# Kernel tuning notes

Hardware: AMD Instinct MI355X
Metric: run time of the kernel (lower is better)

Reference implementation:

```python
import jax, jax.numpy as jnp
import numpy as np

B, L, C, V = 16, 600, 256, 256
OUT_SEQ = 6000
KSZ = 5
DILATIONS = (1, 2, 4)
N_BLOCKS = 10
COND = 256  # speaker(128) + noise(128)
TEMP = 10.0
EPS = 1e-5


def _ccbn(x, cond, gw, gb, bw, bb):
    # x: (B, C, L); conditional batch-norm: per-channel stats over (batch, length),
    # gamma/beta predicted from condition vector.
    mu = jnp.mean(x, axis=(0, 2), keepdims=True)
    var = jnp.var(x, axis=(0, 2), keepdims=True)
    xn = (x - mu) * jax.lax.rsqrt(var + EPS)
    gamma = 1.0 + cond @ gw + gb  # (B, C)
    beta = cond @ bw + bb         # (B, C)
    return xn * gamma[:, :, None] + beta[:, :, None]


def _conv1d(x, w, b, dil=1):
    # x: (B, C_in, L); w: (C_out, C_in, K)
    y = jax.lax.conv_general_dilated(
        x, w, window_strides=(1,), padding='SAME', rhs_dilation=(dil,),
        dimension_numbers=('NCH', 'OIH', 'NCH'))
    return y + b[None, :, None]


def setup_inputs() -> dict:
    key = jax.random.key(0)
    ks = jax.random.split(key, 20)
    s = 0.02
    inp = {
        'inputs': jax.random.randint(ks[0], (B, L), 0, V),
        'speaker_embeddings': jax.random.normal(ks[1], (B, 128), jnp.float32),
        'noise': jax.random.normal(ks[2], (B, 128), jnp.float32),
        'emb': jax.random.normal(ks[3], (V, C), jnp.float32) * s,
        # 10 blocks x 3 dilated convs
        'conv_w': jax.random.normal(ks[4], (N_BLOCKS, 3, C, C, KSZ), jnp.float32) * s,
        'conv_b': jnp.zeros((N_BLOCKS, 3, C), jnp.float32),
        # CCBN projections per conv (gamma/beta from condition)
        'g_w': jax.random.normal(ks[5], (N_BLOCKS, 3, COND, C), jnp.float32) * s,
        'g_b': jnp.zeros((N_BLOCKS, 3, C), jnp.float32),
        'b_w': jax.random.normal(ks[6], (N_BLOCKS, 3, COND, C), jnp.float32) * s,
        'b_b': jnp.zeros((N_BLOCKS, 3, C), jnp.float32),
        # TokenLength head: 2 CCBNs + conv1 (256->256,k1) + conv2 (256->1,k1)
        'tl_g_w': jax.random.normal(ks[7], (2, COND, C), jnp.float32) * s,
        'tl_g_b': jnp.zeros((2, C), jnp.float32),
        'tl_b_w': jax.random.normal(ks[8], (2, COND, C), jnp.float32) * s,
        'tl_b_b': jnp.zeros((2, C), jnp.float32),
        'tl_conv1_w': jax.random.normal(ks[9], (C, C, 1), jnp.float32) * s,
        'tl_conv1_b': jnp.zeros((C,), jnp.float32),
        'tl_conv2_w': jax.random.normal(ks[10], (1, C, 1), jnp.float32) * s,
        'tl_conv2_b': jnp.zeros((1,), jnp.float32),
    }
    return inp


def reference(inputs, speaker_embeddings, noise, emb, conv_w, conv_b,
              g_w, g_b, b_w, b_b, tl_g_w, tl_g_b, tl_b_w, tl_b_b,
              tl_conv1_w, tl_conv1_b, tl_conv2_w, tl_conv2_b):
    cond = jnp.concatenate([speaker_embeddings, noise], axis=-1)  # (B, COND)
    x = emb[inputs]                    # (B, L, C)
    x = jnp.transpose(x, (0, 2, 1))    # (B, C, L)

    # 10 unaligned blocks: residual stacks of CCBN -> ReLU -> dilated conv
    for blk in range(N_BLOCKS):
        y = x
        for j, d in enumerate(DILATIONS):
            y = jax.nn.relu(_ccbn(y, cond, g_w[blk, j], g_b[blk, j], b_w[blk, j], b_b[blk, j]))
            y = _conv1d(y, conv_w[blk, j], conv_b[blk, j], dil=d)
        x = x + y
    unaligned = x  # (B, C, L)

    # TokenLength head
    t = jax.nn.relu(_ccbn(unaligned, cond, tl_g_w[0], tl_g_b[0], tl_b_w[0], tl_b_b[0]))
    t = _conv1d(t, tl_conv1_w, tl_conv1_b)
    t = jax.nn.relu(_ccbn(t, cond, tl_g_w[1], tl_g_b[1], tl_b_w[1], tl_b_b[1]))
    t = _conv1d(t, tl_conv2_w, tl_conv2_b)  # (B, 1, L)
    token_lengths = jax.nn.relu(t[:, 0, :])  # (B, L)

    token_ends = jnp.cumsum(token_lengths, axis=-1)        # (B, L)
    token_centers = token_ends - token_lengths / 2.0        # (B, L)
    aligned_lengths = token_ends

    out_pos = jnp.arange(OUT_SEQ, dtype=jnp.float32)         # (OUT,)
    diff = token_centers[:, None, :] - out_pos[None, :, None]  # (B, OUT, L)
    logits = -(diff * diff) / TEMP
    weights = jax.nn.softmax(logits, axis=-1)                # (B, OUT, L)

    feats = jnp.transpose(unaligned, (0, 2, 1))              # (B, L, C)
    aligned_features = jnp.einsum('bol,blc->boc', weights, feats)  # (B, OUT, C)
    return aligned_features, aligned_lengths
```

## Files before the change

### kernel.cpp

```cpp
#include <hip/hip_runtime.h>
#include <math.h>

#define EPSv 1e-5f

typedef short short8 __attribute__((ext_vector_type(8)));
typedef float floatx4 __attribute__((ext_vector_type(4)));

__device__ __forceinline__ unsigned short f2bf(float x) {
  unsigned u = __float_as_uint(x);
  unsigned r = (u + 0x7fffu + ((u >> 16) & 1u)) >> 16;
  return (unsigned short)r;
}

__global__ void k_zero(float* __restrict__ p) {
  p[blockIdx.x * 256 + threadIdx.x] = 0.f;
}

__global__ void k_gamma_beta(const float* __restrict__ spk, const float* __restrict__ noise,
                             const float* __restrict__ g_w, const float* __restrict__ g_b,
                             const float* __restrict__ b_w, const float* __restrict__ b_b,
                             const float* __restrict__ tl_g_w, const float* __restrict__ tl_g_b,
                             const float* __restrict__ tl_b_w, const float* __restrict__ tl_b_b,
                             float* __restrict__ gammas, float* __restrict__ betas) {
  __shared__ float condl[16*256];
  int t = threadIdx.x;
  for (int idx = t; idx < 4096; idx += 256) {
    int b = idx >> 8, k = idx & 255;
    condl[idx] = (k < 128) ? spk[b*128 + k] : noise[b*128 + k - 128];
  }
  __syncthreads();
  int i = blockIdx.x;
  const float *gw, *bw, *gbias, *bbias;
  if (i < 30) { gw = g_w + (size_t)i*65536; bw = b_w + (size_t)i*65536; gbias = g_b + i*256; bbias = b_b + i*256; }
  else { int j = i - 30; gw = tl_g_w + (size_t)j*65536; bw = tl_b_w + (size_t)j*65536; gbias = tl_g_b + j*256; bbias = tl_b_b + j*256; }
  int co = (t & 63) + blockIdx.y * 64;
  int slot = t >> 6;
  float g[4] = {0.f,0.f,0.f,0.f}, bt[4] = {0.f,0.f,0.f,0.f};
  for (int k = 0; k < 256; ++k) {
    float gwv = gw[k*256 + co];
    float bwv = bw[k*256 + co];
    #pragma unroll
    for (int bb = 0; bb < 4; ++bb) {
      float cv = condl[(slot*4 + bb)*256 + k];
      g[bb]  = fmaf(cv, gwv, g[bb]);
      bt[bb] = fmaf(cv, bwv, bt[bb]);
    }
  }
  #pragma unroll
  for (int bb = 0; bb < 4; ++bb) {
    int b = slot*4 + bb;
    gammas[i*4096 + b*256 + co] = 1.0f + g[bb] + gbias[co];
    betas [i*4096 + b*256 + co] = bt[bb] + bbias[co];
  }
}

template<int TAPS>
__device__ __forceinline__ void wprep_body(const float* __restrict__ src,
                                           unsigned short* __restrict__ dst,
                                           int cotile, int chunk, int t) {
  int cow = t >> 2, ci8 = (t & 3) * 8;
  const float* s0 = src + ((size_t)(cotile*64 + cow)*256 + chunk*32 + ci8)*TAPS;
  float v[8*TAPS];
  #pragma unroll
  for (int i = 0; i < 8*TAPS; ++i) v[i] = s0[i];
  unsigned short* dblk = dst + (size_t)cotile*(8*TAPS*4096) + (size_t)chunk*(TAPS*4096);
  #pragma unroll
  for (int tap = 0; tap < TAPS; ++tap) {
    unsigned hi2[4], lo2[4];
    #pragma unroll
    for (int jj = 0; jj < 4; ++jj) {
      float a = v[(jj*2+0)*TAPS + tap], b = v[(jj*2+1)*TAPS + tap];
      unsigned short ha = f2bf(a), hb = f2bf(b);
      unsigned short la = f2bf(a - __uint_as_float((unsigned)ha << 16));
      unsigned short lb = f2bf(b - __uint_as_float((unsigned)hb << 16));
      hi2[jj] = (unsigned)ha | ((unsigned)hb << 16);
      lo2[jj] = (unsigned)la | ((unsigned)lb << 16);
    }
    uint4 H; H.x = hi2[0]; H.y = hi2[1]; H.z = hi2[2]; H.w = hi2[3];
    uint4 L; L.x = lo2[0]; L.y = lo2[1]; L.z = lo2[2]; L.w = lo2[3];
    *(uint4*)(dblk + (size_t)(tap*2)*2048 + cow*32 + ci8) = H;
    *(uint4*)(dblk + (size_t)(tap*2+1)*2048 + cow*32 + ci8) = L;
  }
}

__global__ __launch_bounds__(256) void k_wprep(const float* __restrict__ conv_w,
                                               const float* __restrict__ tl_c1_w,
                                               unsigned short* __restrict__ wp) {
  int cc = blockIdx.x;
  int cotile = blockIdx.y >> 3, chunk = blockIdx.y & 7;
  if (cc == 30) wprep_body<1>(tl_c1_w, wp + (size_t)30*655360, cotile, chunk, threadIdx.x);
  else          wprep_body<5>(conv_w + (size_t)cc*327680, wp + (size_t)cc*655360, cotile, chunk, threadIdx.x);
}

__global__ void k_embed2(const int* __restrict__ inp, const float* __restrict__ emb,
                         float* __restrict__ x, float* __restrict__ stat0) {
  int bx = blockIdx.x;
  int c = threadIdx.x;
  int r0 = bx * 60;
  float s = 0.f, s2 = 0.f;
  for (int r = 0; r < 60; ++r) {
    int row = inp[r0 + r];
    float v = emb[(size_t)row*256 + c];
    x[(size_t)(r0 + r)*256 + c] = v;
    s += v; s2 = fmaf(v, v, s2);
  }
  atomicAdd(&stat0[c], s);
  atomicAdd(&stat0[256 + c], s2);
}

template<int TAPS>
__global__ __launch_bounds__(256) void k_convm(const float* __restrict__ zin, float* __restrict__ out,
                        const float* __restrict__ stat_in, float* __restrict__ stat_out,
                        const float* __restrict__ gam, const float* __restrict__ bet,
                        const unsigned short* __restrict__ wpc,
                        const float* __restrict__ bias, int dil, int mode) {
  __shared__ unsigned short Zhi[3200];
  __shared__ unsigned short Zlo[3200];
  __shared__ float s_sc[256];
  __shared__ float s_sh[256];
  __shared__ float lsum[32];
  __shared__ float lsq[32];
  int t = threadIdx.x;
  int bx = blockIdx.x;
  int b  = bx / 10;
  int l0 = (bx % 10) * 64;
  int co0 = blockIdx.y * 32;
  int cobase = (blockIdx.y & 1) * 32;
  int PAD = ((TAPS - 1)/2) * dil;
  int ROWS = 64 + 2*PAD;
  int w = t >> 6, lane = t & 63;
  int lsub = (w & 1) * 32, cosub = (w >> 1) * 16;
  int quad = lane >> 4, nlan = lane & 15;
  if (t < 32) { lsum[t] = 0.f; lsq[t] = 0.f; }
  {
    float s = stat_in[t], s2 = stat_in[256 + t];
    float mu = s * (1.0f/9600.0f);
    float var = s2 * (1.0f/9600.0f) - mu*mu;
    float rs = rsqrtf(var + EPSv);
    float scale = rs * gam[b*256 + t];
    s_sc[t] = scale;
    s_sh[t] = fmaf(-mu, scale, bet[b*256 + t]);
  }

  floatx4 acc[2];
  acc[0] = (floatx4){0.f,0.f,0.f,0.f};
  acc[1] = (floatx4){0.f,0.f,0.f,0.f};

  const float* zb = zin + (size_t)b*600*256;
  int srow = t >> 3, fq = t & 7;
  int ar0 = (lsub + nlan) * 40 + quad * 8;
  int ar1 = (lsub + 16 + nlan) * 40 + quad * 8;

  bool va[3]; long zbase[3];
  #pragma unroll
  for (int i = 0; i < 3; ++i) {
    int r = srow + i*32;
    int gl = l0 - PAD + r;
    va[i] = (r < ROWS) && (gl >= 0) && (gl < 600);
    zbase[i] = (long)gl*256 + fq*4;
  }

  for (int chunk = 0; chunk < 8; ++chunk) {
    int ci0 = chunk * 32;
    const unsigned short* pch = wpc + (size_t)((blockIdx.y >> 1)*8 + chunk) * (TAPS*4096);
    short8 bh[TAPS], bl[TAPS];
    int cw = (cobase + cosub + nlan)*32 + quad*8;
    #pragma unroll
    for (int tap = 0; tap < TAPS; ++tap) {
      bh[tap] = *(const short8*)(pch + (size_t)(tap*2)*2048 + cw);
      bl[tap] = *(const short8*)(pch + (size_t)(tap*2+1)*2048 + cw);
    }
    float4 zr[3];
    #pragma unroll
    for (int i = 0; i < 3; ++i) {
      float4 z = {0.f,0.f,0.f,0.f};
      if (va[i]) z = *(const float4*)&zb[zbase[i] + ci0];
      zr[i] = z;
    }
    __syncthreads();
    float4 sc4 = *(const float4*)&s_sc[ci0 + fq*4];
    float4 sh4 = *(const float4*)&s_sh[ci0 + fq*4];
    #pragma unroll
    for (int i = 0; i < 3; ++i) {
      int r = srow + i*32;
      if (r < ROWS) {
        float4 z = zr[i];
        bool inr = va[i];
        float v0 = inr ? fmaxf(fmaf(z.x, sc4.x, sh4.x), 0.f) : 0.f;
        float v1 = inr ? fmaxf(fmaf(z.y, sc4.y, sh4.y), 0.f) : 0.f;
        float v2 = inr ? fmaxf(fmaf(z.z, sc4.z, sh4.z), 0.f) : 0.f;
        float v3 = inr ? fmaxf(fmaf(z.w, sc4.w, sh4.w), 0.f) : 0.f;
        unsigned short h0 = f2bf(v0), h1 = f2bf(v1), h2 = f2bf(v2), h3 = f2bf(v3);
        unsigned short e0 = f2bf(v0 - __uint_as_float((unsigned)h0 << 16));
        unsigned short e1 = f2bf(v1 - __uint_as_float((unsigned)h1 << 16));
        unsigned short e2 = f2bf(v2 - __uint_as_float((unsigned)h2 << 16));
        unsigned short e3 = f2bf(v3 - __uint_as_float((unsigned)h3 << 16));
        uint2 vh; vh.x = (unsigned)h0 | ((unsigned)h1 << 16);
        vh.y = (unsigned)h2 | ((unsigned)h3 << 16);
        uint2 vl; vl.x = (unsigned)e0 | ((unsigned)e1 << 16);
        vl.y = (unsigned)e2 | ((unsigned)e3 << 16);
        *(uint2*)&Zhi[r*40 + fq*4] = vh;
        *(uint2*)&Zlo[r*40 + fq*4] = vl;
      }
    }
    __syncthreads();
    #pragma unroll
    for (int tap = 0; tap < TAPS; ++tap) {
      int sh = tap * dil * 40;
      short8 ah0 = *(const short8*)&Zhi[ar0 + sh];
      short8 ah1 = *(const short8*)&Zhi[ar1 + sh];
      short8 al0 = *(const short8*)&Zlo[ar0 + sh];
      short8 al1 = *(const short8*)&Zlo[ar1 + sh];
      acc[0] = __builtin_amdgcn_mfma_f32_16x16x32_bf16(ah0, bh[tap], acc[0], 0, 0, 0);
      acc[0] = __builtin_amdgcn_mfma_f32_16x16x32_bf16(ah0, bl[tap], acc[0], 0, 0, 0);
      acc[0] = __builtin_amdgcn_mfma_f32_16x16x32_bf16(al0, bh[tap], acc[0], 0, 0, 0);
      acc[1] = __builtin_amdgcn_mfma_f32_16x16x32_bf16(ah1, bh[tap], acc[1], 0, 0, 0);
      acc[1] = __builtin_amdgcn_mfma_f32_16x16x32_bf16(ah1, bl[tap], acc[1], 0, 0, 0);
      acc[1] = __builtin_amdgcn_mfma_f32_16x16x32_bf16(al1, bh[tap], acc[1], 0, 0, 0);
    }
  }

  float bsv = bias[co0 + cosub + nlan];
  float ssum = 0.f, ssq = 0.f;
  #pragma unroll
  for (int mt = 0; mt < 2; ++mt) {
    #pragma unroll
    for (int r = 0; r < 4; ++r) {
      int l = l0 + lsub + mt*16 + quad*4 + r;
      if (l < 600) {
        float v = acc[mt][r] + bsv;
        float* dst = &out[((size_t)(b*600 + l))*256 + co0 + cosub + nlan];
        if (mode) v += *dst;
        *dst = v;
        ssum += v;
        ssq = fmaf(v, v, ssq);
      }
    }
  }
  ssum += __shfl_xor(ssum, 16, 64);
  ssum += __shfl_xor(ssum, 32, 64);
  ssq  += __shfl_xor(ssq, 16, 64);
  ssq  += __shfl_xor(ssq, 32, 64);
  if (quad == 0) {
    atomicAdd(&lsum[cosub + nlan], ssum);
    atomicAdd(&lsq [cosub + nlan], ssq);
  }
  __syncthreads();
  if (t < 32) {
    atomicAdd(&stat_out[co0 + t], lsum[t]);
    atomicAdd(&stat_out[256 + co0 + t], lsq[t]);
  }
}

__global__ void k_tl2(const float* __restrict__ z, const float* __restrict__ stat,
                      const float* __restrict__ gam, const float* __restrict__ bet,
                      const float* __restrict__ w2, const float* __restrict__ b2,
                      float* __restrict__ tl) {
  int t = threadIdx.x;
  int row = blockIdx.x * 4 + (t >> 6);
  int lane = t & 63;
  int b = row / 600;
  float4 s1 = *(const float4*)&stat[lane*4];
  float4 s2 = *(const float4*)&stat[256 + lane*4];
  float4 gm = *(const float4*)&gam[b*256 + lane*4];
  float4 bt = *(const float4*)&bet[b*256 + lane*4];
  float sc[4], sh[4];
  {
    float sv[4] = {s1.x, s1.y, s1.z, s1.w};
    float qv[4] = {s2.x, s2.y, s2.z, s2.w};
    float gv[4] = {gm.x, gm.y, gm.z, gm.w};
    float bv[4] = {bt.x, bt.y, bt.z, bt.w};
    #pragma unroll
    for (int i = 0; i < 4; ++i) {
      float mu = sv[i] * (1.0f/9600.0f);
      float var = qv[i] * (1.0f/9600.0f) - mu*mu;
      float rs = rsqrtf(var + EPSv);
      sc[i] = rs * gv[i];
      sh[i] = fmaf(-mu, sc[i], bv[i]);
    }
  }
  float4 zr = *(const float4*)&z[(size_t)row*256 + lane*4];
  float4 wr = *(const float4*)&w2[lane*4];
  float z0 = fmaxf(fmaf(zr.x, sc[0], sh[0]), 0.f);
  float z1 = fmaxf(fmaf(zr.y, sc[1], sh[1]), 0.f);
  float z2 = fmaxf(fmaf(zr.z, sc[2], sh[2]), 0.f);
  float z3 = fmaxf(fmaf(zr.w, sc[3], sh[3]), 0.f);
  float s = z0*wr.x + z1*wr.y + z2*wr.z + z3*wr.w;
  for (int m = 32; m >= 1; m >>= 1) s += __shfl_xor(s, m, 64);
  if (lane == 0) tl[row] = fmaxf(s + b2[0], 0.f);
}

__global__ void k_cumsum(const float* __restrict__ tl, float* __restrict__ centers,
                         float* __restrict__ out_len) {
  int b = blockIdx.x; int lane = threadIdx.x;
  float carry = 0.f;
  for (int ch = 0; ch < 10; ++ch) {
    int l = ch*64 + lane;
    float v = (l < 600) ? tl[b*600 + l] : 0.f;
    float s = v;
    #pragma unroll
    for (int off = 1; off < 64; off <<= 1) {
      float n = __shfl_up(s, off, 64);
      if (lane >= off) s += n;
    }
    float ends = carry + s;
    if (l < 600) {
      centers[b*600 + l] = ends - 0.5f*v;
      out_len[b*600 + l] = ends;
    }
    carry = __shfl(ends, 63, 64);
  }
}

__global__ void k_tobf16(const float* __restrict__ x, unsigned short* __restrict__ fbT) {
  __shared__ unsigned short T[64*66];
  int b = blockIdx.x, lt = blockIdx.y, ct = blockIdx.z;
  int t = threadIdx.x;
  int i4 = t >> 6;
  int j = t & 63;
  #pragma unroll
  for (int r = 0; r < 16; ++r) {
    int li = i4*16 + r;
    int l = lt*64 + li;
    float v = (l < 600) ? x[((size_t)(b*600 + l))*256 + ct*64 + j] : 0.f;
    T[j*66 + li] = f2bf(v);
  }
  __syncthreads();
  int row = t >> 2, seg = (t & 3) * 16;
  unsigned vv[8];
  #pragma unroll
  for (int k = 0; k < 8; ++k)
    vv[k] = *(const unsigned*)&T[row*66 + seg + k*2];
  size_t dsth = ((size_t)(b*256 + ct*64 + row))*640 + lt*64 + seg;
  unsigned* du = (unsigned*)fbT;
  uint4 a; a.x = vv[0]; a.y = vv[1]; a.z = vv[2]; a.w = vv[3];
  uint4 c4; c4.x = vv[4]; c4.y = vv[5]; c4.z = vv[6]; c4.w = vv[7];
  *(uint4*)(du + dsth/2) = a;
  *(uint4*)(du + dsth/2 + 4) = c4;
}

__global__ __launch_bounds__(256) void k_align2(const unsigned short* __restrict__ fbT,
                        const float* __restrict__ centers, float* __restrict__ outp) {
  __shared__ float cen[600];
  __shared__ float mrow[64];
  __shared__ float isum[64];
  __shared__ unsigned short Wt[64*72];
  __shared__ unsigned short Ft[256*72];
  int b = blockIdx.x;
  int o0 = blockIdx.y * 64;
  int t = threadIdx.x;
  int wv = t >> 6, lane = t & 63;
  for (int i = t; i < 600; i += 256) cen[i] = centers[b*600 + i];
  __syncthreads();
  for (int rr = 0; rr < 16; ++rr) {
    int oi = wv*16 + rr;
    float opos = (float)(o0 + oi);
    float mx = -3.0e38f;
    for (int l = lane; l < 600; l += 64) {
      float d = cen[l] - opos;
      mx = fmaxf(mx, -d*d*0.1f);
    }
    #pragma unroll
    for (int mm = 32; mm >= 1; mm >>= 1) mx = fmaxf(mx, __shfl_xor(mx, mm, 64));
    if (lane == 0) mrow[oi] = mx;
  }
  __syncthreads();
  floatx4 acc[4][4];
  #pragma unroll
  for (int i = 0; i < 4; ++i)
    #pragma unroll
    for (int j = 0; j < 4; ++j)
      acc[i][j] = (floatx4){0.f, 0.f, 0.f, 0.f};
  int quad = lane >> 4;
  int nlan = lane & 15;
  int oi_w = t >> 2;
  int sbase = t & 3;
  float mo = mrow[oi_w];
  float opos_w = (float)(o0 + oi_w);
  float psum = 0.f;
  const unsigned short* srcb = fbT + ((size_t)b*256)*640;

  for (int ch = 0; ch < 10; ++ch) {
    int lc0 = ch * 64;
    __syncthreads();
    #pragma unroll
    for (int sidx = 0; sidx < 2; ++sidx) {
      int seg = sbase + sidx*4;
      unsigned pk[4];
      #pragma unroll
      for (int jj = 0; jj < 8; jj += 2) {
        int li = lc0 + seg*8 + jj;
        float e0 = 0.f, e1 = 0.f;
        if (li < 600)     { float d = cen[li] - opos_w;     e0 = __expf(-d*d*0.1f - mo); }
        if (li + 1 < 600) { float d = cen[li + 1] - opos_w; e1 = __expf(-d*d*0.1f - mo); }
        psum += e0 + e1;
        pk[jj>>1] = (unsigned)f2bf(e0) | ((unsigned)f2bf(e1) << 16);
      }
      uint4 v; v.x = pk[0]; v.y = pk[1]; v.z = pk[2]; v.w = pk[3];
      *(uint4*)&Wt[oi_w*72 + seg*8] = v;
    }
    #pragma unroll
    for (int it = 0; it < 8; ++it) {
      int idx = t + it*256;
      int c = idx >> 3, part = idx & 7;
      uint4 v = *(const uint4*)(srcb + (size_t)c*640 + lc0 + part*8);
      *(uint4*)&Ft[c*72 + part*8] = v;
    }
    __syncthreads();
    #pragma unroll
    for (int ks = 0; ks < 2; ++ks) {
      int ko = ks*32 + quad*8;
      short8 af[4], bfr[4];
      #pragma unroll
      for (int mt = 0; mt < 4; ++mt)
        af[mt] = *(const short8*)&Wt[(mt*16 + nlan)*72 + ko];
      #pragma unroll
      for (int nt = 0; nt < 4; ++nt)
        bfr[nt] = *(const short8*)&Ft[(wv*64 + nt*16 + nlan)*72 + ko];
      #pragma unroll
      for (int mt = 0; mt < 4; ++mt)
        #pragma unroll
        for (int nt = 0; nt < 4; ++nt)
          acc[mt][nt] = __builtin_amdgcn_mfma_f32_16x16x32_bf16(af[mt], bfr[nt], acc[mt][nt], 0, 0, 0);
    }
  }
  psum += __shfl_xor(psum, 1, 64);
  psum += __shfl_xor(psum, 2, 64);
  if ((t & 3) == 0) isum[oi_w] = 1.0f / psum;
  __syncthreads();
  #pragma unroll
  for (int mt = 0; mt < 4; ++mt) {
    #pragma unroll
    for (int r = 0; r < 4; ++r) {
      int oi = mt*16 + quad*4 + r;
      int o = o0 + oi;
      if (o < 6000) {
        float sc = isum[oi];
        #pragma unroll
        for (int nt = 0; nt < 4; ++nt) {
          int c = wv*64 + nt*16 + nlan;
          outp[((size_t)b*6000 + o)*256 + c] = acc[mt][nt][r] * sc;
        }
      }
    }
  }
}

extern "C" void kernel_launch(void* const* d_in, const int* in_sizes, int n_in,
                              void* d_out, int out_size, void* d_ws, size_t ws_size,
                              hipStream_t stream) {
  const int*   inputs = (const int*)  d_in[0];
  const float* spk    = (const float*)d_in[1];
  const float* noise  = (const float*)d_in[2];
  const float* emb    = (const float*)d_in[3];
  const float* conv_w = (const float*)d_in[4];
  const float* conv_b = (const float*)d_in[5];
  const float* g_w    = (const float*)d_in[6];
  const float* g_b    = (const float*)d_in[7];
  const float* b_w    = (const float*)d_in[8];
  const float* b_b    = (const float*)d_in[9];
  const float* tl_g_w = (const float*)d_in[10];
  const float* tl_g_b = (const float*)d_in[11];
  const float* tl_b_w = (const float*)d_in[12];
  const float* tl_b_b = (const float*)d_in[13];
  const float* tl_c1_w = (const float*)d_in[14];
  const float* tl_c1_b = (const float*)d_in[15];
  const float* tl_c2_w = (const float*)d_in[16];
  const float* tl_c2_b = (const float*)d_in[17];
  float* out = (float*)d_out;

  float* ws = (float*)d_ws;
  float* x       = ws;
  float* A       = x + 2457600;
  float* Bf      = A + 2457600;
  float* gammas  = Bf + 2457600;
  float* betas   = gammas + 131072;
  float* statacc = betas + 131072;
  float* tl      = statacc + 16384;
  float* cen     = tl + 9600;
  unsigned short* wp = (unsigned short*)(cen + 9600);
  unsigned short* fbT = (unsigned short*)Bf;

  k_zero<<<dim3(64), dim3(256), 0, stream>>>(statacc);
  k_wprep<<<dim3(31, 32), dim3(256), 0, stream>>>(conv_w, tl_c1_w, wp);
  k_gamma_beta<<<dim3(32, 4), dim3(256), 0, stream>>>(spk, noise, g_w, g_b, b_w, b_b,
      tl_g_w, tl_g_b, tl_b_w, tl_b_b, gammas, betas);
  k_embed2<<<dim3(160), dim3(256), 0, stream>>>(inputs, emb, x, statacc);

  const int dils[3] = {1, 2, 4};
  for (int blk = 0; blk < 10; ++blk) {
    const float* srcs[3] = {x, A, Bf};
    float*       dsts[3] = {A, Bf, x};
    for (int j = 0; j < 3; ++j) {
      int idx = blk*3 + j;
      int mode = (j == 2) ? 1 : 0;
      k_convm<5><<<dim3(160, 8), dim3(256), 0, stream>>>(srcs[j], dsts[j],
          statacc + idx*512, statacc + (idx+1)*512,
          gammas + idx*4096, betas + idx*4096,
          wp + (size_t)idx*655360, conv_b + idx*256, dils[j], mode);
    }
  }
  k_convm<1><<<dim3(160, 8), dim3(256), 0, stream>>>(x, A,
      statacc + 30*512, statacc + 31*512,
      gammas + 30*4096, betas + 30*4096,
      wp + (size_t)30*655360, tl_c1_b, 1, 0);
  k_tl2<<<dim3(2400), dim3(256), 0, stream>>>(A, statacc + 31*512,
      gammas + 31*4096, betas + 31*4096, tl_c2_w, tl_c2_b, tl);
  k_cumsum<<<dim3(16), dim3(64), 0, stream>>>(tl, cen, out + 24576000);
  k_tobf16<<<dim3(16, 10, 4), dim3(256), 0, stream>>>(x, fbT);
  k_align2<<<dim3(16, 94), dim3(256), 0, stream>>>(fbT, cen, out);
}
```

Baseline: 1.655 ms.

## Replace 4-wave conv blocks with single-wave 32x32 tiles without barriers

The dilated conv kernel moves from 256-thread blocks covering 64 positions by 32 output channels to one-wavefront blocks covering 32 positions by 32 channels. Each wave now computes a 2x2 grid of MFMA tiles, which raises register-level reuse of the activation and weight fragments. Because the block is a single wave, all __syncthreads and the shared-memory reduction of the statistics are dropped, and the grid grows to many more blocks. In exchange, the halo rows form a larger share of each staged tile, global loads are no longer issued ahead of the staging step, and correctness now relies on in-order LDS behaviour within one wave.

```diff
diff --git a/kernel.cpp b/kernel.cpp
--- a/kernel.cpp
+++ b/kernel.cpp
@@ -109,101 +109,76 @@
 }
 
 template<int TAPS>
-__global__ __launch_bounds__(256) void k_convm(const float* __restrict__ zin, float* __restrict__ out,
+__global__ __launch_bounds__(64, 4) void k_convw(const float* __restrict__ zin, float* __restrict__ out,
                         const float* __restrict__ stat_in, float* __restrict__ stat_out,
                         const float* __restrict__ gam, const float* __restrict__ bet,
                         const unsigned short* __restrict__ wpc,
                         const float* __restrict__ bias, int dil, int mode) {
-  __shared__ unsigned short Zhi[3200];
-  __shared__ unsigned short Zlo[3200];
+  __shared__ unsigned short Zhi[48*40];
+  __shared__ unsigned short Zlo[48*40];
   __shared__ float s_sc[256];
   __shared__ float s_sh[256];
-  __shared__ float lsum[32];
-  __shared__ float lsq[32];
-  int t = threadIdx.x;
+  int lane = threadIdx.x;
   int bx = blockIdx.x;
-  int b  = bx / 10;
-  int l0 = (bx % 10) * 64;
+  int b = bx / 19, lt = bx % 19;
+  int l0 = lt * 32;
   int co0 = blockIdx.y * 32;
-  int cobase = (blockIdx.y & 1) * 32;
-  int PAD = ((TAPS - 1)/2) * dil;
-  int ROWS = 64 + 2*PAD;
-  int w = t >> 6, lane = t & 63;
-  int lsub = (w & 1) * 32, cosub = (w >> 1) * 16;
+  int PAD = ((TAPS - 1) / 2) * dil;
+  int ROWS = 32 + 2 * PAD;
   int quad = lane >> 4, nlan = lane & 15;
-  if (t < 32) { lsum[t] = 0.f; lsq[t] = 0.f; }
-  {
-    float s = stat_in[t], s2 = stat_in[256 + t];
+  #pragma unroll
+  for (int i = 0; i < 4; ++i) {
+    int c = lane + i * 64;
+    float s = stat_in[c], s2 = stat_in[256 + c];
     float mu = s * (1.0f/9600.0f);
     float var = s2 * (1.0f/9600.0f) - mu*mu;
     float rs = rsqrtf(var + EPSv);
-    float scale = rs * gam[b*256 + t];
-    s_sc[t] = scale;
-    s_sh[t] = fmaf(-mu, scale, bet[b*256 + t]);
-  }
-
-  floatx4 acc[2];
-  acc[0] = (floatx4){0.f,0.f,0.f,0.f};
-  acc[1] = (floatx4){0.f,0.f,0.f,0.f};
+    float scale = rs * gam[b*256 + c];
+    s_sc[c] = scale;
+    s_sh[c] = fmaf(-mu, scale, bet[b*256 + c]);
+  }
+
+  floatx4 acc[2][2];
+  #pragma unroll
+  for (int i = 0; i < 2; ++i)
+    #pragma unroll
+    for (int j = 0; j < 2; ++j) acc[i][j] = (floatx4){0.f,0.f,0.f,0.f};
 
   const float* zb = zin + (size_t)b*600*256;
-  int srow = t >> 3, fq = t & 7;
-  int ar0 = (lsub + nlan) * 40 + quad * 8;
-  int ar1 = (lsub + 16 + nlan) * 40 + quad * 8;
-
-  bool va[3]; long zbase[3];
-  #pragma unroll
-  for (int i = 0; i < 3; ++i) {
-    int r = srow + i*32;
-    int gl = l0 - PAD + r;
-    va[i] = (r < ROWS) && (gl >= 0) && (gl < 600);
-    zbase[i] = (long)gl*256 + fq*4;
-  }
+  int srow = lane >> 3, fq = lane & 7;
+  int ar0 = nlan*40 + quad*8;
+  int ar1 = ar0 + 16*40;
+  const unsigned short* wbase = wpc + (size_t)(blockIdx.y >> 1) * 8 * (TAPS*4096);
+  int cob = (blockIdx.y & 1) * 32;
+  int cw0 = (cob + nlan)*32 + quad*8;
+  int cw1 = cw0 + 512;
 
   for (int chunk = 0; chunk < 8; ++chunk) {
     int ci0 = chunk * 32;
-    const unsigned short* pch = wpc + (size_t)((blockIdx.y >> 1)*8 + chunk) * (TAPS*4096);
-    short8 bh[TAPS], bl[TAPS];
-    int cw = (cobase + cosub + nlan)*32 + quad*8;
-    #pragma unroll
-    for (int tap = 0; tap < TAPS; ++tap) {
-      bh[tap] = *(const short8*)(pch + (size_t)(tap*2)*2048 + cw);
-      bl[tap] = *(const short8*)(pch + (size_t)(tap*2+1)*2048 + cw);
-    }
-    float4 zr[3];
-    #pragma unroll
-    for (int i = 0; i < 3; ++i) {
-      float4 z = {0.f,0.f,0.f,0.f};
-      if (va[i]) z = *(const float4*)&zb[zbase[i] + ci0];
-      zr[i] = z;
-    }
-    __syncthreads();
     float4 sc4 = *(const float4*)&s_sc[ci0 + fq*4];
     float4 sh4 = *(const float4*)&s_sh[ci0 + fq*4];
-    #pragma unroll
-    for (int i = 0; i < 3; ++i) {
-      int r = srow + i*32;
-      if (r < ROWS) {
-        float4 z = zr[i];
-        bool inr = va[i];
-        float v0 = inr ? fmaxf(fmaf(z.x, sc4.x, sh4.x), 0.f) : 0.f;
-        float v1 = inr ? fmaxf(fmaf(z.y, sc4.y, sh4.y), 0.f) : 0.f;
-        float v2 = inr ? fmaxf(fmaf(z.z, sc4.z, sh4.z), 0.f) : 0.f;
-        float v3 = inr ? fmaxf(fmaf(z.w, sc4.w, sh4.w), 0.f) : 0.f;
-        unsigned short h0 = f2bf(v0), h1 = f2bf(v1), h2 = f2bf(v2), h3 = f2bf(v3);
-        unsigned short e0 = f2bf(v0 - __uint_as_float((unsigned)h0 << 16));
-        unsigned short e1 = f2bf(v1 - __uint_as_float((unsigned)h1 << 16));
-        unsigned short e2 = f2bf(v2 - __uint_as_float((unsigned)h2 << 16));
-        unsigned short e3 = f2bf(v3 - __uint_as_float((unsigned)h3 << 16));
-        uint2 vh; vh.x = (unsigned)h0 | ((unsigned)h1 << 16);
-        vh.y = (unsigned)h2 | ((unsigned)h3 << 16);
-        uint2 vl; vl.x = (unsigned)e0 | ((unsigned)e1 << 16);
-        vl.y = (unsigned)e2 | ((unsigned)e3 << 16);
-        *(uint2*)&Zhi[r*40 + fq*4] = vh;
-        *(uint2*)&Zlo[r*40 + fq*4] = vl;
-      }
-    }
-    __syncthreads();
+    for (int r = srow; r < ROWS; r += 8) {
+      int gl = l0 - PAD + r;
+      bool inr = (gl >= 0 && gl < 600);
+      float4 z = {0.f,0.f,0.f,0.f};
+      if (inr) z = *(const float4*)&zb[(size_t)gl*256 + ci0 + fq*4];
+      float v0 = inr ? fmaxf(fmaf(z.x, sc4.x, sh4.x), 0.f) : 0.f;
+      float v1 = inr ? fmaxf(fmaf(z.y, sc4.y, sh4.y), 0.f) : 0.f;
+      float v2 = inr ? fmaxf(fmaf(z.z, sc4.z, sh4.z), 0.f) : 0.f;
+      float v3 = inr ? fmaxf(fmaf(z.w, sc4.w, sh4.w), 0.f) : 0.f;
+      unsigned short h0 = f2bf(v0), h1 = f2bf(v1), h2 = f2bf(v2), h3 = f2bf(v3);
+      unsigned short e0 = f2bf(v0 - __uint_as_float((unsigned)h0 << 16));
+      unsigned short e1 = f2bf(v1 - __uint_as_float((unsigned)h1 << 16));
+      unsigned short e2 = f2bf(v2 - __uint_as_float((unsigned)h2 << 16));
+      unsigned short e3 = f2bf(v3 - __uint_as_float((unsigned)h3 << 16));
+      uint2 vh; vh.x = (unsigned)h0 | ((unsigned)h1 << 16);
+      vh.y = (unsigned)h2 | ((unsigned)h3 << 16);
+      uint2 vl; vl.x = (unsigned)e0 | ((unsigned)e1 << 16);
+      vl.y = (unsigned)e2 | ((unsigned)e3 << 16);
+      *(uint2*)&Zhi[r*40 + fq*4] = vh;
+      *(uint2*)&Zlo[r*40 + fq*4] = vl;
+    }
+    const unsigned short* pch = wbase + (size_t)chunk * (TAPS*4096);
     #pragma unroll
     for (int tap = 0; tap < TAPS; ++tap) {
       int sh = tap * dil * 40;
@@ -211,44 +186,58 @@
       short8 ah1 = *(const short8*)&Zhi[ar1 + sh];
       short8 al0 = *(const short8*)&Zlo[ar0 + sh];
       short8 al1 = *(const short8*)&Zlo[ar1 + sh];
-      acc[0] = __builtin_amdgcn_mfma_f32_16x16x32_bf16(ah0, bh[tap], acc[0], 0, 0, 0);
-      acc[0] = __builtin_amdgcn_mfma_f32_16x16x32_bf16(ah0, bl[tap], acc[0], 0, 0, 0);
-      acc[0] = __builtin_amdgcn_mfma_f32_16x16x32_bf16(al0, bh[tap], acc[0], 0, 0, 0);
-      acc[1] = __builtin_amdgcn_mfma_f32_16x16x32_bf16(ah1, bh[tap], acc[1], 0, 0, 0);
-      acc[1] = __builtin_amdgcn_mfma_f32_16x16x32_bf16(ah1, bl[tap], acc[1], 0, 0, 0);
-      acc[1] = __builtin_amdgcn_mfma_f32_16x16x32_bf16(al1, bh[tap], acc[1], 0, 0, 0);
-    }
-  }
-
-  float bsv = bias[co0 + cosub + nlan];
-  float ssum = 0.f, ssq = 0.f;
+      const unsigned short* pt = pch + (size_t)(tap*2)*2048;
+      short8 bh0 = *(const short8*)(pt + cw0);
+      short8 bh1 = *(const short8*)(pt + cw1);
+      short8 bl0 = *(const short8*)(pt + 2048 + cw0);
+      short8 bl1 = *(const short8*)(pt + 2048 + cw1);
+      acc[0][0] = __builtin_amdgcn_mfma_f32_16x16x32_bf16(ah0, bh0, acc[0][0], 0, 0, 0);
+      acc[0][0] = __builtin_amdgcn_mfma_f32_16x16x32_bf16(ah0, bl0, acc[0][0], 0, 0, 0);
+      acc[0][0] = __builtin_amdgcn_mfma_f32_16x16x32_bf16(al0, bh0, acc[0][0], 0, 0, 0);
+      acc[0][1] = __builtin_amdgcn_mfma_f32_16x16x32_bf16(ah0, bh1, acc[0][1], 0, 0, 0);
+      acc[0][1] = __builtin_amdgcn_mfma_f32_16x16x32_bf16(ah0, bl1, acc[0][1], 0, 0, 0);
+      acc[0][1] = __builtin_amdgcn_mfma_f32_16x16x32_bf16(al0, bh1, acc[0][1], 0, 0, 0);
+      acc[1][0] = __builtin_amdgcn_mfma_f32_16x16x32_bf16(ah1, bh0, acc[1][0], 0, 0, 0);
+      acc[1][0] = __builtin_amdgcn_mfma_f32_16x16x32_bf16(ah1, bl0, acc[1][0], 0, 0, 0);
+      acc[1][0] = __builtin_amdgcn_mfma_f32_16x16x32_bf16(al1, bh0, acc[1][0], 0, 0, 0);
+      acc[1][1] = __builtin_amdgcn_mfma_f32_16x16x32_bf16(ah1, bh1, acc[1][1], 0, 0, 0);
+      acc[1][1] = __builtin_amdgcn_mfma_f32_16x16x32_bf16(ah1, bl1, acc[1][1], 0, 0, 0);
+      acc[1][1] = __builtin_amdgcn_mfma_f32_16x16x32_bf16(al1, bh1, acc[1][1], 0, 0, 0);
+    }
+  }
+
+  float bsv0 = bias[co0 + nlan];
+  float bsv1 = bias[co0 + 16 + nlan];
+  float ssum0 = 0.f, ssq0 = 0.f, ssum1 = 0.f, ssq1 = 0.f;
   #pragma unroll
   for (int mt = 0; mt < 2; ++mt) {
     #pragma unroll
     for (int r = 0; r < 4; ++r) {
-      int l = l0 + lsub + mt*16 + quad*4 + r;
+      int l = l0 + mt*16 + quad*4 + r;
       if (l < 600) {
-        float v = acc[mt][r] + bsv;
-        float* dst = &out[((size_t)(b*600 + l))*256 + co0 + cosub + nlan];
-        if (mode) v += *dst;
-        *dst = v;
-        ssum += v;
-        ssq = fmaf(v, v, ssq);
+        size_t rowo = ((size_t)(b*600 + l))*256 + co0;
+        float v0 = acc[mt][0][r] + bsv0;
+        float* d0 = &out[rowo + nlan];
+        if (mode) v0 += *d0;
+        *d0 = v0;
+        ssum0 += v0; ssq0 = fmaf(v0, v0, ssq0);
+        float v1 = acc[mt][1][r] + bsv1;
+        float* d1 = &out[rowo + 16 + nlan];
+        if (mode) v1 += *d1;
+        *d1 = v1;
+        ssum1 += v1; ssq1 = fmaf(v1, v1, ssq1);
       }
     }
   }
-  ssum += __shfl_xor(ssum, 16, 64);
-  ssum += __shfl_xor(ssum, 32, 64);
-  ssq  += __shfl_xor(ssq, 16, 64);
-  ssq  += __shfl_xor(ssq, 32, 64);
+  ssum0 += __shfl_xor(ssum0, 16, 64); ssum0 += __shfl_xor(ssum0, 32, 64);
+  ssq0  += __shfl_xor(ssq0, 16, 64);  ssq0  += __shfl_xor(ssq0, 32, 64);
+  ssum1 += __shfl_xor(ssum1, 16, 64); ssum1 += __shfl_xor(ssum1, 32, 64);
+  ssq1  += __shfl_xor(ssq1, 16, 64);  ssq1  += __shfl_xor(ssq1, 32, 64);
   if (quad == 0) {
-    atomicAdd(&lsum[cosub + nlan], ssum);
-    atomicAdd(&lsq [cosub + nlan], ssq);
-  }
-  __syncthreads();
-  if (t < 32) {
-    atomicAdd(&stat_out[co0 + t], lsum[t]);
-    atomicAdd(&stat_out[256 + co0 + t], lsq[t]);
+    atomicAdd(&stat_out[co0 + nlan], ssum0);
+    atomicAdd(&stat_out[256 + co0 + nlan], ssq0);
+    atomicAdd(&stat_out[co0 + 16 + nlan], ssum1);
+    atomicAdd(&stat_out[256 + co0 + 16 + nlan], ssq1);
   }
 }
 
@@ -494,13 +483,13 @@
     for (int j = 0; j < 3; ++j) {
       int idx = blk*3 + j;
       int mode = (j == 2) ? 1 : 0;
-      k_convm<5><<<dim3(160, 8), dim3(256), 0, stream>>>(srcs[j], dsts[j],
+      k_convw<5><<<dim3(304, 8), dim3(64), 0, stream>>>(srcs[j], dsts[j],
           statacc + idx*512, statacc + (idx+1)*512,
           gammas + idx*4096, betas + idx*4096,
           wp + (size_t)idx*655360, conv_b + idx*256, dils[j], mode);
     }
   }
-  k_convm<1><<<dim3(160, 8), dim3(256), 0, stream>>>(x, A,
+  k_convw<1><<<dim3(304, 8), dim3(64), 0, stream>>>(x, A,
       statacc + 30*512, statacc + 31*512,
       gammas + 30*4096, betas + 30*4096,
       wp + (size_t)30*655360, tl_c1_b, 1, 0);
```

New measurement: 1.784 ms. 7.8% more time.
